# Optimization experiments

Hardware: AMD Instinct MI355X
Metric: run time of the kernel (lower is better)

Reference implementation:

```python
import jax, jax.numpy as jnp
import numpy as np


def _gru_cell(h, x, Wih, Whh, bih, bhh):
    # PyTorch GRU cell, gate order (r, z, n)
    gi = x @ Wih.T + bih      # [B, 3H]
    gh = h @ Whh.T + bhh      # [B, 3H]
    i_r, i_z, i_n = jnp.split(gi, 3, axis=-1)
    h_r, h_z, h_n = jnp.split(gh, 3, axis=-1)
    r = jax.nn.sigmoid(i_r + h_r)
    z = jax.nn.sigmoid(i_z + h_z)
    n = jnp.tanh(i_n + r * h_n)
    return (1.0 - z) * n + z * h


def _run_gru(xs, h0, Wih, Whh, bih, bhh):
    # xs: [T, B, E] -> (h_T [B, H], outputs [T, B, H])
    def step(h, x):
        h = _gru_cell(h, x, Wih, Whh, bih, bhh)
        return h, h
    return jax.lax.scan(step, h0, xs)


def setup_inputs() -> dict:
    key = jax.random.key(0)
    ks = jax.random.split(key, 14)
    V, E, H1, H2, W, C = 101, 512, 1024, 1024, 2048, 24

    def p(k, shape, fan):
        return jax.random.normal(k, shape, jnp.float32) / np.float32(np.sqrt(fan))

    return {
        "x": jax.random.randint(ks[0], (1, W, C), 0, V),
        "emb": p(ks[1], (V, E), E),
        "Wih1": p(ks[2], (3 * H1, E), E),
        "Whh1": p(ks[3], (3 * H1, H1), H1),
        "bih1": jnp.zeros((3 * H1,), jnp.float32),
        "bhh1": jnp.zeros((3 * H1,), jnp.float32),
        "Wih2f": p(ks[4], (3 * H2, H1), H1),
        "Whh2f": p(ks[5], (3 * H2, H2), H2),
        "bih2f": jnp.zeros((3 * H2,), jnp.float32),
        "bhh2f": jnp.zeros((3 * H2,), jnp.float32),
        "Wih2b": p(ks[6], (3 * H2, H1), H1),
        "Whh2b": p(ks[7], (3 * H2, H2), H2),
        "bih2b": jnp.zeros((3 * H2,), jnp.float32),
        "bhh2b": jnp.zeros((3 * H2,), jnp.float32),
    }


def reference(x, emb, Wih1, Whh1, bih1, bhh1,
              Wih2f, Whh2f, bih2f, bhh2f,
              Wih2b, Whh2b, bih2b, bhh2b):
    # x: [1, W, C] int indices. Dropout is treated as eval-mode (identity).
    Wn = x.shape[1]
    H1 = Whh1.shape[1]
    H2 = Whh2f.shape[1]

    e = emb[x[0]]                       # [W, C, E]
    xs = jnp.transpose(e, (1, 0, 2))    # [C, W, E] -- words batched together
    h0 = jnp.zeros((Wn, H1), e.dtype)
    word_emb, _ = _run_gru(xs, h0, Wih1, Whh1, bih1, bhh1)  # final hidden == last output

    # word-level bidirectional GRU, batch size 1 (the sentence)
    ws = word_emb[:, None, :]           # [W, 1, H1]
    h0w = jnp.zeros((1, H2), e.dtype)
    _, fwd = _run_gru(ws, h0w, Wih2f, Whh2f, bih2f, bhh2f)          # [W, 1, H2]
    _, bwd = _run_gru(ws[::-1], h0w, Wih2b, Whh2b, bih2b, bhh2b)    # reversed
    ctx = jnp.concatenate([fwd[:, 0, :], bwd[::-1][:, 0, :]], axis=-1)  # [W, 2*H2]

    return word_emb[None], ctx[None]    # ([1, W, H1], [1, W, 2*H2])
```

## Files before the change

### kernel.cpp

```cpp
#include <hip/hip_runtime.h>

typedef unsigned short u16;
typedef unsigned int   u32;
typedef unsigned long long u64;
typedef long long      i64;
typedef __attribute__((ext_vector_type(8))) short  short8;
typedef __attribute__((ext_vector_type(8))) __bf16 bf16x8;
typedef __attribute__((ext_vector_type(4))) float  f32x4;

#define W_N   2048
#define C_N   24
#define E_N   512
#define H_N   1024
#define G3_N  3072
#define CH    256
#define SEG   512
#define NBLK  64
#define COLS  16
#define SENT  0xFFFFFFFFu

#define MD_BF16 0u
#define MD_F32  1u
#define MD_ZERO 2u

__device__ inline float bf2f(u16 u) { union { u32 i; float f; } v; v.i = ((u32)u) << 16; return v.f; }
__device__ inline u16 f2bf(float f) {
  union { float f; u32 i; } v; v.f = f;
  u32 i = v.i;
  u32 r = (i + 0x7fffu + ((i >> 16) & 1u)) >> 16;
  return (u16)r;
}
__device__ inline float ld1(const void* p, size_t eoff, u32 md) {
  if (md == MD_F32) return ((const float*)p)[eoff];
  if (md == MD_ZERO) return 0.f;
  return bf2f(((const u16*)p)[eoff]);
}
__device__ inline short8 ld8(const void* p, size_t eoff, u32 md) {
  short8 r;
  if (md == MD_BF16) return *(const short8*)((const u16*)p + eoff);
  if (md == MD_ZERO) {
#pragma unroll
    for (int i = 0; i < 8; ++i) r[i] = 0;
    return r;
  }
  const float* f = (const float*)p + eoff;
#pragma unroll
  for (int i = 0; i < 8; ++i) r[i] = (short)f2bf(f[i]);
  return r;
}

__device__ inline void split8(f32x4 v0, f32x4 v1, bf16x8& hi, bf16x8& lo) {
#pragma unroll
  for (int i = 0; i < 4; ++i) {
    float f = v0[i];
    __bf16 h = (__bf16)f;
    hi[i] = h;
    lo[i] = (__bf16)(f - (float)h);
  }
#pragma unroll
  for (int i = 0; i < 4; ++i) {
    float f = v1[i];
    __bf16 h = (__bf16)f;
    hi[4 + i] = h;
    lo[4 + i] = (__bf16)(f - (float)h);
  }
}

__device__ inline void ldsplit(const void* p, size_t eoff, u32 md,
                               bf16x8& hi, bf16x8& lo) {
  if (md == MD_F32) {
    const float* f = (const float*)p + eoff;
    f32x4 v0 = *(const f32x4*)f;
    f32x4 v1 = *(const f32x4*)(f + 4);
    split8(v0, v1, hi, lo);
  } else if (md == MD_BF16) {
    union { short8 s; bf16x8 b; } u;
    u.s = *(const short8*)((const u16*)p + eoff);
    hi = u.b;
#pragma unroll
    for (int i = 0; i < 8; ++i) lo[i] = (__bf16)0.f;
  } else {
#pragma unroll
    for (int i = 0; i < 8; ++i) { hi[i] = (__bf16)0.f; lo[i] = (__bf16)0.f; }
  }
}

struct PtrPack { const void* p[14]; };

__global__ void sniffall_kernel(PtrPack pk, u32* __restrict__ flags) {
  if (threadIdx.x != 0) return;
  const int b = blockIdx.x;
  if (b == 0) {
    const int* xi = (const int*)pk.p[0];
    int oddzero = 0;
    for (int i = 0; i < 128; ++i)
      if (xi[2 * i + 1] == 0) oddzero++;
    flags[0] = (oddzero >= 120) ? 1u : 0u;
  } else {
    const u16* t = (const u16*)pk.p[b];
    int cnt = 0, nz = 0;
    for (int i = 0; i < 512; ++i) {
      u32 v = t[i];
      if (v != 0u) nz++;
      u32 e = (v >> 7) & 0xffu;
      if (e >= 100u && e <= 130u) cnt++;
    }
    flags[b] = (nz == 0) ? MD_ZERO : ((cnt >= 440) ? MD_BF16 : MD_F32);
  }
}

#define SWZ(row, kc) (((row) << 6) + ((kc) ^ (((row) & 7) << 3)))

template<int GATHER>
__global__ __launch_bounds__(256)
void mgemm_kernel(const void* __restrict__ A, const void* __restrict__ Wt,
                  const void* __restrict__ bias, float* __restrict__ Cout,
                  const void* __restrict__ X, int xoff, int gstride, int K,
                  const u32* __restrict__ flags, int afi, int wfi, int bfi,
                  int m_base) {
  __shared__ u16 AhS[64 * 64], AlS[64 * 64], BhS[64 * 64], BlS[64 * 64];
  __shared__ int arowS[64];
  const u32 am = (afi == -1) ? MD_BF16 : ((afi == -2) ? MD_F32 : flags[afi]);
  const u32 wm = flags[wfi];
  const u32 bm = flags[bfi];
  const int tid = threadIdx.x;
  const int bn0 = blockIdx.x * 64, bm0 = blockIdx.y * 64;
  if (GATHER) {
    if (tid < 64) {
      const int ar = m_base + bm0 + tid;
      int ix = flags[0] ? (int)((const i64*)X)[(size_t)ar * gstride + xoff]
                        : ((const int*)X)[(size_t)ar * gstride + xoff];
      arowS[tid] = min(max(ix, 0), 100);
    }
    __syncthreads();
  }
  const int wave = tid >> 6, lane = tid & 63;
  const int wr = (wave >> 1) * 32, wc = (wave & 1) * 32;
  const bool loA = (am == MD_F32), loB = (wm == MD_F32);

  f32x4 acc[2][2];
#pragma unroll
  for (int i = 0; i < 2; ++i)
#pragma unroll
    for (int j = 0; j < 2; ++j)
#pragma unroll
      for (int r = 0; r < 4; ++r) acc[i][j][r] = 0.f;

  for (int k0 = 0; k0 < K; k0 += 64) {
#pragma unroll
    for (int i = 0; i < 2; ++i) {
      const int ch = tid + i * 256;
      const int row = ch >> 3, kc = (ch & 7) * 8;
      {
        const int grow = GATHER ? arowS[row] : (m_base + bm0 + row);
        bf16x8 hi, lo;
        ldsplit(A, (size_t)grow * K + k0 + kc, am, hi, lo);
        const int o = SWZ(row, kc);
        *(bf16x8*)&AhS[o] = hi;
        *(bf16x8*)&AlS[o] = lo;
      }
      {
        bf16x8 hi, lo;
        ldsplit(Wt, (size_t)(bn0 + row) * K + k0 + kc, wm, hi, lo);
        const int o = SWZ(row, kc);
        *(bf16x8*)&BhS[o] = hi;
        *(bf16x8*)&BlS[o] = lo;
      }
    }
    __syncthreads();
#pragma unroll
    for (int ks = 0; ks < 64; ks += 32) {
      bf16x8 ah[2], al[2], bh[2], bl[2];
      const int lr = lane & 15, lk = ks + (lane >> 4) * 8;
#pragma unroll
      for (int i = 0; i < 2; ++i) {
        ah[i] = *(const bf16x8*)&AhS[SWZ(wr + i * 16 + lr, lk)];
        al[i] = *(const bf16x8*)&AlS[SWZ(wr + i * 16 + lr, lk)];
        bh[i] = *(const bf16x8*)&BhS[SWZ(wc + i * 16 + lr, lk)];
        bl[i] = *(const bf16x8*)&BlS[SWZ(wc + i * 16 + lr, lk)];
      }
#pragma unroll
      for (int i = 0; i < 2; ++i)
#pragma unroll
        for (int j = 0; j < 2; ++j) {
          acc[i][j] = __builtin_amdgcn_mfma_f32_16x16x32_bf16(ah[i], bh[j], acc[i][j], 0, 0, 0);
          if (loA)
            acc[i][j] = __builtin_amdgcn_mfma_f32_16x16x32_bf16(al[i], bh[j], acc[i][j], 0, 0, 0);
          if (loB)
            acc[i][j] = __builtin_amdgcn_mfma_f32_16x16x32_bf16(ah[i], bl[j], acc[i][j], 0, 0, 0);
        }
    }
    __syncthreads();
  }
  const int lr = lane & 15, m4 = (lane >> 4) * 4;
#pragma unroll
  for (int j = 0; j < 2; ++j) {
    const int n = bn0 + wc + j * 16 + lr;
    const float bv = ld1(bias, n, bm);
#pragma unroll
    for (int i = 0; i < 2; ++i) {
      const int m = bm0 + wr + i * 16 + m4;
#pragma unroll
      for (int r = 0; r < 4; ++r)
        Cout[(size_t)(m + r) * G3_N + n] = acc[i][j][r] + bv;
    }
  }
}

__device__ inline void seg_pass(
    const void* __restrict__ A, u32 am, int gather, const int* arowS, int bm0,
    const void* __restrict__ Wt, u32 wm, int bn0, int K,
    int tid, int wave, int lane,
    u16* AhS, u16* AlS, u16* B0h, u16* B0l, u16* B1h, u16* B1l, u16* B2h, u16* B2l,
    f32x4 (&aR)[2][2], f32x4 (&aZ)[2][2], f32x4 (&aN)[2][2]) {
  const bool loA = (am == MD_F32), loB = (wm == MD_F32);
  u16* BhS[3] = {B0h, B1h, B2h};
  u16* BlS[3] = {B0l, B1l, B2l};
  const int wr = (wave >> 1) * 32, wc = (wave & 1) * 32;
  for (int k0 = 0; k0 < K; k0 += 64) {
    __syncthreads();
#pragma unroll
    for (int i = 0; i < 2; ++i) {
      const int ch = tid + i * 256;
      const int row = ch >> 3, kc = (ch & 7) * 8;
      const int grow = gather ? arowS[row] : (bm0 + row);
      bf16x8 hi, lo;
      ldsplit(A, (size_t)grow * K + k0 + kc, am, hi, lo);
      const int o = SWZ(row, kc);
      *(bf16x8*)&AhS[o] = hi;
      *(bf16x8*)&AlS[o] = lo;
#pragma unroll
      for (int g = 0; g < 3; ++g) {
        bf16x8 bhi, blo;
        ldsplit(Wt, (size_t)(g * 1024 + bn0 + row) * K + k0 + kc, wm, bhi, blo);
        *(bf16x8*)&BhS[g][o] = bhi;
        *(bf16x8*)&BlS[g][o] = blo;
      }
    }
    __syncthreads();
#pragma unroll
    for (int ks = 0; ks < 64; ks += 32) {
      const int lr = lane & 15, lk = ks + (lane >> 4) * 8;
      bf16x8 ah[2], al[2];
#pragma unroll
      for (int i = 0; i < 2; ++i) {
        ah[i] = *(const bf16x8*)&AhS[SWZ(wr + i * 16 + lr, lk)];
        al[i] = *(const bf16x8*)&AlS[SWZ(wr + i * 16 + lr, lk)];
      }
#pragma unroll
      for (int g = 0; g < 3; ++g) {
        bf16x8 bh[2], bl[2];
#pragma unroll
        for (int j = 0; j < 2; ++j) {
          bh[j] = *(const bf16x8*)&BhS[g][SWZ(wc + j * 16 + lr, lk)];
          bl[j] = *(const bf16x8*)&BlS[g][SWZ(wc + j * 16 + lr, lk)];
        }
        f32x4 (&acc)[2][2] = (g == 0) ? aR : (g == 1) ? aZ : aN;
#pragma unroll
        for (int i = 0; i < 2; ++i)
#pragma unroll
          for (int j = 0; j < 2; ++j) {
            acc[i][j] = __builtin_amdgcn_mfma_f32_16x16x32_bf16(ah[i], bh[j], acc[i][j], 0, 0, 0);
            if (loA)
              acc[i][j] = __builtin_amdgcn_mfma_f32_16x16x32_bf16(al[i], bh[j], acc[i][j], 0, 0, 0);
            if (loB)
              acc[i][j] = __builtin_amdgcn_mfma_f32_16x16x32_bf16(ah[i], bl[j], acc[i][j], 0, 0, 0);
          }
      }
    }
  }
}

__global__ __launch_bounds__(256)
void fgru_kernel(const void* __restrict__ emb, const void* __restrict__ Wih,
                 const void* __restrict__ bih, const void* __restrict__ Whh,
                 const void* __restrict__ bhh,
                 const float* __restrict__ hin, float* __restrict__ hout,
                 float* __restrict__ wout,
                 const void* __restrict__ X, int xoff, int gstride,
                 const u32* __restrict__ flags) {
  __shared__ u16 AhS[64 * 64], AlS[64 * 64];
  __shared__ u16 B0h[64 * 64], B0l[64 * 64];
  __shared__ u16 B1h[64 * 64], B1l[64 * 64];
  __shared__ u16 B2h[64 * 64], B2l[64 * 64];
  __shared__ int arowS[64];
  const u32 amE = flags[1], wmI = flags[2], wmH = flags[3];
  const u32 bmI = flags[4], bmH = flags[5];
  const int tid = threadIdx.x, wave = tid >> 6, lane = tid & 63;
  const int bn0 = blockIdx.x * 64;
  const int bm0 = blockIdx.y * 64;
  if (tid < 64) {
    const int ar = bm0 + tid;
    int ix = flags[0] ? (int)((const i64*)X)[(size_t)ar * gstride + xoff]
                      : ((const int*)X)[(size_t)ar * gstride + xoff];
    arowS[tid] = min(max(ix, 0), 100);
  }

  f32x4 aR[2][2], aZ[2][2], aIN[2][2], aHN[2][2];
#pragma unroll
  for (int i = 0; i < 2; ++i)
#pragma unroll
    for (int j = 0; j < 2; ++j)
#pragma unroll
      for (int r = 0; r < 4; ++r) {
        aR[i][j][r] = 0.f; aZ[i][j][r] = 0.f;
        aIN[i][j][r] = 0.f; aHN[i][j][r] = 0.f;
      }

  seg_pass(emb, amE, 1, arowS, bm0, Wih, wmI, bn0, E_N,
           tid, wave, lane, AhS, AlS, B0h, B0l, B1h, B1l, B2h, B2l, aR, aZ, aIN);
  seg_pass(hin, MD_F32, 0, arowS, bm0, Whh, wmH, bn0, H_N,
           tid, wave, lane, AhS, AlS, B0h, B0l, B1h, B1l, B2h, B2l, aR, aZ, aHN);

  const int wr = (wave >> 1) * 32, wc = (wave & 1) * 32;
  const int lr = lane & 15, m4 = (lane >> 4) * 4;
#pragma unroll
  for (int j = 0; j < 2; ++j) {
    const int n = bn0 + wc + j * 16 + lr;
    const float biR = ld1(bih, n, bmI),        bhR = ld1(bhh, n, bmH);
    const float biZ = ld1(bih, 1024 + n, bmI), bhZ = ld1(bhh, 1024 + n, bmH);
    const float biN = ld1(bih, 2048 + n, bmI), bhN = ld1(bhh, 2048 + n, bmH);
#pragma unroll
    for (int i = 0; i < 2; ++i) {
      const int m = bm0 + wr + i * 16 + m4;
#pragma unroll
      for (int r4 = 0; r4 < 4; ++r4) {
        const size_t off = (size_t)(m + r4) * H_N + n;
        const float rg = 1.f / (1.f + expf(-(aR[i][j][r4] + biR + bhR)));
        const float zg = 1.f / (1.f + expf(-(aZ[i][j][r4] + biZ + bhZ)));
        const float ng = tanhf(aIN[i][j][r4] + biN + rg * (aHN[i][j][r4] + bhN));
        const float ho = (1.f - zg) * ng + zg * hin[off];
        hout[off] = ho;
        if (wout) wout[off] = ho;
      }
    }
  }
}

__global__ __launch_bounds__(256)
void gru_cell_kernel(const float* __restrict__ gi, const float* __restrict__ gh,
                     float* __restrict__ hf, float* __restrict__ wout, int mb) {
  const int idx = blockIdx.x * 256 + threadIdx.x;
  const int m = idx >> 10, j = idx & 1023;
  const float* gim = gi + (size_t)m * G3_N;
  const float* ghm = gh + (size_t)m * G3_N;
  const float ir = gim[j], iz = gim[1024 + j], inn = gim[2048 + j];
  const float hr = ghm[j], hz = ghm[1024 + j], hn = ghm[2048 + j];
  const float r = 1.f / (1.f + expf(-(ir + hr)));
  const float z = 1.f / (1.f + expf(-(iz + hz)));
  const float n = tanhf(inn + r * hn);
  const float ho = (1.f - z) * n + z * hf[idx];
  hf[idx] = ho;
  if (wout) wout[(size_t)(mb + m) * H_N + j] = ho;
}

__device__ void mgemm_body(const float* __restrict__ A, const void* __restrict__ Wt,
                           const void* __restrict__ bias, float* __restrict__ Cout,
                           u32 wm, u32 bm, int bm0, int bn0, char* smem, int tid) {
  u16* AhS = (u16*)smem;
  u16* AlS = AhS + 4096;
  u16* BhS = AlS + 4096;
  u16* BlS = BhS + 4096;
  const int wave = tid >> 6, lane = tid & 63;
  const int wr = (wave >> 1) * 32, wc = (wave & 1) * 32;
  const bool loB = (wm == MD_F32);
  const int K = H_N;

  f32x4 acc[2][2];
#pragma unroll
  for (int i = 0; i < 2; ++i)
#pragma unroll
    for (int j = 0; j < 2; ++j)
#pragma unroll
      for (int r = 0; r < 4; ++r) acc[i][j][r] = 0.f;

  for (int k0 = 0; k0 < K; k0 += 64) {
#pragma unroll
    for (int i = 0; i < 2; ++i) {
      const int ch = tid + i * 256;
      const int row = ch >> 3, kc = (ch & 7) * 8;
      {
        bf16x8 hi, lo;
        ldsplit(A, (size_t)(bm0 + row) * K + k0 + kc, MD_F32, hi, lo);
        const int o = SWZ(row, kc);
        *(bf16x8*)&AhS[o] = hi;
        *(bf16x8*)&AlS[o] = lo;
      }
      {
        bf16x8 hi, lo;
        ldsplit(Wt, (size_t)(bn0 + row) * K + k0 + kc, wm, hi, lo);
        const int o = SWZ(row, kc);
        *(bf16x8*)&BhS[o] = hi;
        *(bf16x8*)&BlS[o] = lo;
      }
    }
    __syncthreads();
#pragma unroll
    for (int ks = 0; ks < 64; ks += 32) {
      bf16x8 ah[2], al[2], bh[2], bl[2];
      const int lr = lane & 15, lk = ks + (lane >> 4) * 8;
#pragma unroll
      for (int i = 0; i < 2; ++i) {
        ah[i] = *(const bf16x8*)&AhS[SWZ(wr + i * 16 + lr, lk)];
        al[i] = *(const bf16x8*)&AlS[SWZ(wr + i * 16 + lr, lk)];
        bh[i] = *(const bf16x8*)&BhS[SWZ(wc + i * 16 + lr, lk)];
        bl[i] = *(const bf16x8*)&BlS[SWZ(wc + i * 16 + lr, lk)];
      }
#pragma unroll
      for (int i = 0; i < 2; ++i)
#pragma unroll
        for (int j = 0; j < 2; ++j) {
          acc[i][j] = __builtin_amdgcn_mfma_f32_16x16x32_bf16(ah[i], bh[j], acc[i][j], 0, 0, 0);
          acc[i][j] = __builtin_amdgcn_mfma_f32_16x16x32_bf16(al[i], bh[j], acc[i][j], 0, 0, 0);
          if (loB)
            acc[i][j] = __builtin_amdgcn_mfma_f32_16x16x32_bf16(ah[i], bl[j], acc[i][j], 0, 0, 0);
        }
    }
    __syncthreads();
  }
  const int lr = lane & 15, m4 = (lane >> 4) * 4;
#pragma unroll
  for (int j = 0; j < 2; ++j) {
    const int n = bn0 + wc + j * 16 + lr;
    const float bv = ld1(bias, n, bm);
#pragma unroll
    for (int i = 0; i < 2; ++i) {
      const int m = bm0 + wr + i * 16 + m4;
#pragma unroll
      for (int r = 0; r < 4; ++r) {
        union { float f; u32 u; } cv; cv.f = acc[i][j][r] + bv;
        __hip_atomic_store((u32*)Cout + (size_t)(m + r) * G3_N + n, cv.u,
                           __ATOMIC_RELAXED, __HIP_MEMORY_SCOPE_AGENT);
      }
    }
  }
}

__device__ void seq_body(const void* __restrict__ Whh, const void* __restrict__ bhh,
                         const float* __restrict__ gi, float* __restrict__ ctx,
                         u32 wm, u32 bm, int dir, int blk, char* smem, int tid,
                         int nsteps) {
  u16* wsh = (u16*)smem;
  const int dirofs = dir << 10;
  const int wave = tid >> 6, lane = tid & 63;
  const int j0 = blk * COLS;
  const int jw = wave * 4;

  for (int e = tid * 8; e < 48 * 1024; e += 256 * 8) {
    const int lr = e >> 10, col = e & 1023;
    const int g = lr >> 4, jj = lr & 15;
    *(short8*)&wsh[e] = ld8(Whh, (size_t)(g * 1024 + j0 + jj) * 1024 + col, wm);
  }
  float br = 0.f, bz = 0.f, bn = 0.f;
  if (lane < 4) {
    br = ld1(bhh, 0 * 1024 + j0 + jw + lane, bm);
    bz = ld1(bhh, 1 * 1024 + j0 + jw + lane, bm);
    bn = ld1(bhh, 2 * 1024 + j0 + jw + lane, bm);
  }
  __syncthreads();

  float hp = 0.f;
  for (int t = 0; t < nsteps; ++t) {
    const int row = dir ? (nsteps - 1 - t) : t;
    u32 ga = 0, gb = 0, gc = 0;
    {
      const u32* gp = (const u32*)(gi + (size_t)row * G3_N + (j0 + jw + (lane & 3)));
      for (;;) {
        if (lane < 4) {
          ga = __hip_atomic_load(gp,        __ATOMIC_RELAXED, __HIP_MEMORY_SCOPE_AGENT);
          gb = __hip_atomic_load(gp + 1024, __ATOMIC_RELAXED, __HIP_MEMORY_SCOPE_AGENT);
          gc = __hip_atomic_load(gp + 2048, __ATOMIC_RELAXED, __HIP_MEMORY_SCOPE_AGENT);
        }
        const bool bad = (lane < 4) && (ga == SENT || gb == SENT || gc == SENT);
        if (__ballot(bad) == 0ull) break;
      }
    }
    union { u32 u; float f; } c0, c1, c2;
    c0.u = ga; c1.u = gb; c2.u = gc;
    const float ir = c0.f, iz = c1.f, inn = c2.f;

    float hreg[16];
    if (t == 0) {
#pragma unroll
      for (int i = 0; i < 16; ++i) hreg[i] = 0.f;
    } else {
      const int prow = dir ? (nsteps - t) : (t - 1);
      const u64* hsrc = (const u64*)(ctx + (size_t)prow * 2048 + dirofs);
      u64 hv[8];
      for (;;) {
        bool bad = false;
#pragma unroll
        for (int c = 0; c < 8; ++c) {
          hv[c] = __hip_atomic_load(hsrc + c * 64 + lane,
                                    __ATOMIC_RELAXED, __HIP_MEMORY_SCOPE_AGENT);
          if ((u32)hv[c] == SENT || (u32)(hv[c] >> 32) == SENT)
            bad = true;
        }
        if (__ballot(bad) == 0ull) break;
      }
#pragma unroll
      for (int c = 0; c < 8; ++c) {
        union { u64 u; float f[2]; } cv; cv.u = hv[c];
        hreg[2 * c]     = cv.f[0];
        hreg[2 * c + 1] = cv.f[1];
      }
    }
    float sv[12];
#pragma unroll
    for (int g = 0; g < 3; ++g)
#pragma unroll
      for (int jj = 0; jj < 4; ++jj) {
        const u32* wrow = (const u32*)&wsh[(g * 16 + jw + jj) * 1024];
        float s = 0.f;
#pragma unroll
        for (int c = 0; c < 8; ++c) {
          const u32 u = wrow[c * 64 + lane];
          union { u32 i; float f; } lo2, hi2;
          lo2.i = u << 16; hi2.i = u & 0xffff0000u;
          s = fmaf(lo2.f, hreg[2 * c], s);
          s = fmaf(hi2.f, hreg[2 * c + 1], s);
        }
#pragma unroll
        for (int off = 32; off > 0; off >>= 1) s += __shfl_xor(s, off);
        sv[g * 4 + jj] = s;
      }
    if (lane < 4) {
      const float hr = (lane == 0 ? sv[0] : lane == 1 ? sv[1] : lane == 2 ? sv[2] : sv[3]) + br;
      const float hz = (lane == 0 ? sv[4] : lane == 1 ? sv[5] : lane == 2 ? sv[6] : sv[7]) + bz;
      const float hn = (lane == 0 ? sv[8] : lane == 1 ? sv[9] : lane == 2 ? sv[10] : sv[11]) + bn;
      const float r = 1.f / (1.f + expf(-(ir + hr)));
      const float z = 1.f / (1.f + expf(-(iz + hz)));
      const float n = tanhf(inn + r * hn);
      const float ho = (1.f - z) * n + z * hp;
      hp = ho;
      union { float f; u32 i; } v; v.f = ho;
      __hip_atomic_store((u32*)(ctx + (size_t)row * 2048) + dirofs + j0 + jw + lane,
                         v.i, __ATOMIC_RELAXED, __HIP_MEMORY_SCOPE_AGENT);
    }
  }
}

__global__ __launch_bounds__(256)
void p2_kernel(const void* __restrict__ Whf, const void* __restrict__ bhf,
               const void* __restrict__ Whb, const void* __restrict__ bhb,
               const void* __restrict__ Wif, const void* __restrict__ bif,
               const void* __restrict__ Wib, const void* __restrict__ bib,
               const float* __restrict__ wemb, float* __restrict__ G0,
               float* __restrict__ G1, float* __restrict__ ctx,
               const u32* __restrict__ flags, int nsteps) {
  __shared__ __align__(16) char smem[48 * 1024 * 2];
  const int tid = threadIdx.x;
  const int bid = blockIdx.x;
  if (bid < 2 * NBLK) {
    const int dir = bid >> 6, blk = bid & 63;
    seq_body(dir ? Whb : Whf, dir ? bhb : bhf, dir ? G1 : G0, ctx,
             flags[dir ? 11 : 7], flags[dir ? 13 : 9], dir, blk, smem, tid, nsteps);
  } else {
    int b = bid - 2 * NBLK;
    if (b < 1536) {
      const int bx = b % 48, by = b / 48;
      mgemm_body(wemb, Wif, bif, G0, flags[6], flags[8], by * 64, bx * 64, smem, tid);
    } else {
      b -= 1536;
      const int bx = b % 48, by = 31 - (b / 48);
      mgemm_body(wemb, Wib, bib, G1, flags[10], flags[12], by * 64, bx * 64, smem, tid);
    }
  }
}

__global__ __launch_bounds__(256)
void seq_kernel(const void* __restrict__ Whh, const void* __restrict__ bhh,
                const float* __restrict__ gi, float* hb, unsigned* cnt,
                float* __restrict__ ctx, const u32* __restrict__ flags,
                int wfi, int bfi, int word_base, int rev, int dirofs) {
  const u32 wm = flags[wfi], bm = flags[bfi];
  const int blk = blockIdx.x;
  const int tid = threadIdx.x;
  const int wave = tid >> 6, lane = tid & 63;
  const int j0 = blk * 8;

  __shared__ __align__(16) u16 wsh[24 * 1024];
  __shared__ float hshf[1024];
  __shared__ float ghs[24];
  __shared__ float bhs[24];
  __shared__ float hnew[8];

  for (int e = tid * 8; e < 24 * 1024; e += 256 * 8) {
    const int lr = e >> 10, col = e & 1023;
    const int g = lr >> 3, jj = lr & 7;
    *(short8*)&wsh[e] = ld8(Whh, (size_t)(g * 1024 + j0 + jj) * 1024 + col, wm);
  }
  if (tid < 24) bhs[tid] = ld1(bhh, (tid >> 3) * 1024 + j0 + (tid & 7), bm);
  __syncthreads();

  unsigned target = 0;
  for (int t = 0; t < SEG; ++t) {
    const int row = rev ? (SEG - 1 - t) : t;
    const int wt = word_base + row;
    const u32* hsrc = (const u32*)(hb + (t & 1) * 1024);
    u32* hdst = (u32*)hshf;
    if (wave == 0) {
#pragma unroll
      for (int c = 0; c < 16; ++c)
        hdst[c * 64 + lane] = __hip_atomic_load(hsrc + c * 64 + lane,
                                                __ATOMIC_RELAXED, __HIP_MEMORY_SCOPE_AGENT);
    }
    __syncthreads();
    float hreg[16];
#pragma unroll
    for (int c = 0; c < 8; ++c) {
      const int kp = 2 * (c * 64 + lane);
      hreg[2 * c]     = hshf[kp];
      hreg[2 * c + 1] = hshf[kp + 1];
    }
#pragma unroll
    for (int q = 0; q < 6; ++q) {
      const int lr = wave * 6 + q;
      const u32* wrow = (const u32*)&wsh[lr * 1024];
      float s = 0.f;
#pragma unroll
      for (int c = 0; c < 8; ++c) {
        const u32 u = wrow[c * 64 + lane];
        union { u32 i; float f; } lo, hi;
        lo.i = u << 16; hi.i = u & 0xffff0000u;
        s = fmaf(lo.f, hreg[2 * c], s);
        s = fmaf(hi.f, hreg[2 * c + 1], s);
      }
#pragma unroll
      for (int off = 32; off > 0; off >>= 1) s += __shfl_xor(s, off);
      if (lane == 0) ghs[lr] = s;
    }
    __syncthreads();
    if (tid < 8) {
      const int jj = tid;
      const float hr = ghs[jj] + bhs[jj];
      const float hz = ghs[8 + jj] + bhs[8 + jj];
      const float hn = ghs[16 + jj] + bhs[16 + jj];
      const float* gim = gi + (size_t)row * G3_N + (j0 + jj);
      const float ir = gim[0], iz = gim[1024], inn = gim[2048];
      const float r = 1.f / (1.f + expf(-(ir + hr)));
      const float z = 1.f / (1.f + expf(-(iz + hz)));
      const float n = tanhf(inn + r * hn);
      const float hp = hshf[j0 + jj];
      const float ho = (1.f - z) * n + z * hp;
      ctx[(size_t)wt * 2048 + dirofs + j0 + jj] = ho;
      hnew[jj] = ho;
    }
    __syncthreads();
    if (tid < 8) {
      union { float f; u32 i; } v; v.f = hnew[tid];
      __hip_atomic_store((u32*)(hb + ((t + 1) & 1) * 1024) + blk * 8 + tid, v.i,
                         __ATOMIC_RELAXED, __HIP_MEMORY_SCOPE_AGENT);
    }
    target += 128;
    if (tid == 0) {
      __hip_atomic_fetch_add(cnt, 1u, __ATOMIC_RELEASE, __HIP_MEMORY_SCOPE_AGENT);
      while (__hip_atomic_load(cnt, __ATOMIC_ACQUIRE, __HIP_MEMORY_SCOPE_AGENT) < target)
        __builtin_amdgcn_s_sleep(2);
    }
    __syncthreads();
  }
}

extern "C" void kernel_launch(void* const* d_in, const int* in_sizes, int n_in,
                              void* d_out, int out_size, void* d_ws, size_t ws_size,
                              hipStream_t stream) {
  char* w = (char*)d_ws;
  u32* flags = (u32*)(w);
  float* hbuf = (float*)(w + 1024);
  const size_t GBASE = 20480;

  hipMemsetAsync(w, 0, GBASE, stream);

  PtrPack pk;
  for (int i = 0; i < 14; ++i) pk.p[i] = d_in[i];
  sniffall_kernel<<<14, 64, 0, stream>>>(pk, flags);

  float* wemb = (float*)d_out;
  float* ctx  = (float*)d_out + (size_t)W_N * H_N;

  const size_t SZ_G  = (size_t)W_N * G3_N * 4;
  const size_t SZ_HF = (size_t)W_N * H_N * 4;
  const size_t needA = GBASE + 2 * SZ_G + SZ_HF;

  if (ws_size >= needA) {
    float* G0 = (float*)(w + GBASE);
    float* G1 = (float*)(w + GBASE + SZ_G);
    float* HA = (float*)(w + GBASE + 2 * SZ_G);
    float* HB = G0;

    hipMemsetAsync(HA, 0, SZ_HF, stream);

    float* bufs[2] = {HA, HB};
    dim3 gf(H_N / 64, W_N / 64);
    for (int c = 0; c < C_N; ++c) {
      fgru_kernel<<<gf, 256, 0, stream>>>(d_in[1], d_in[2], d_in[4], d_in[3], d_in[5],
                                          bufs[c & 1], bufs[(c + 1) & 1],
                                          (c == C_N - 1) ? wemb : (float*)nullptr,
                                          d_in[0], c, C_N, flags);
    }

    hipMemsetAsync(G0, 0xFF, SZ_G, stream);
    hipMemsetAsync(G1, 0xFF, SZ_G, stream);
    hipMemsetAsync(ctx, 0xFF, (size_t)W_N * 2048 * 4, stream);

    p2_kernel<<<2 * NBLK + 2 * 1536, 256, 0, stream>>>(
        d_in[7], d_in[9], d_in[11], d_in[13],
        d_in[6], d_in[8], d_in[10], d_in[12],
        wemb, G0, G1, ctx, flags, W_N);
  } else {
    float* G0  = (float*)(w + GBASE);
    float* GIc = G0;
    float* GHc = G0 + (size_t)CH * G3_N;
    float* HF  = (float*)(w + GBASE + (size_t)SEG * G3_N * 4);

    dim3 g1(G3_N / 64, CH / 64);
    for (int chk = 0; chk < W_N / CH; ++chk) {
      const int mb = chk * CH;
      hipMemsetAsync(HF, 0, (size_t)CH * H_N * 4, stream);
      for (int c = 0; c < C_N; ++c) {
        mgemm_kernel<1><<<g1, 256, 0, stream>>>(d_in[1], d_in[2], d_in[4], GIc,
                                                d_in[0], c, C_N, E_N, flags, 1, 2, 4, mb);
        mgemm_kernel<0><<<g1, 256, 0, stream>>>(HF, d_in[3], d_in[5], GHc,
                                                nullptr, 0, 0, H_N, flags, -2, 3, 5, 0);
        gru_cell_kernel<<<(CH * H_N) / 256, 256, 0, stream>>>(
            GIc, GHc, HF, (c == C_N - 1) ? wemb : (float*)nullptr, mb);
      }
    }
    dim3 g2(G3_N / 64, SEG / 64);
    for (int s = 0; s < W_N / SEG; ++s) {
      mgemm_kernel<0><<<g2, 256, 0, stream>>>(wemb, d_in[6], d_in[8], G0,
                                              nullptr, 0, 0, H_N, flags, -2, 6, 8, s * SEG);
      seq_kernel<<<128, 256, 0, stream>>>(d_in[7], d_in[9], G0, hbuf,
                                          (unsigned*)(w + 64 + (0 * 4 + s) * 64),
                                          ctx, flags, 7, 9, s * SEG, 0, 0);
    }
    for (int s = W_N / SEG - 1; s >= 0; --s) {
      mgemm_kernel<0><<<g2, 256, 0, stream>>>(wemb, d_in[10], d_in[12], G0,
                                              nullptr, 0, 0, H_N, flags, -2, 10, 12, s * SEG);
      seq_kernel<<<128, 256, 0, stream>>>(d_in[11], d_in[13], G0, hbuf + 2048,
                                          (unsigned*)(w + 64 + (1 * 4 + s) * 64),
                                          ctx, flags, 11, 13, s * SEG, 1, 1024);
    }
  }
}
```

Measured before the change: 9.880 ms.

## Precompute embedding-input projection table over vocabulary and gather it per step

Since the vocabulary has only 101 entries, the input projection emb·Wih^T + bih is computed once into a 128x3072 table by a gather-mode GEMM. Each of the 24 char-level GRU steps then looks up rows of this table instead of redoing a K=512 GEMM against the embedding. This removes roughly a third of the per-step matrix work and the Wih weight streaming. In exchange it adds one small GEMM launch and scattered table reads in the epilogue.

```diff
diff --git a/kernel.cpp b/kernel.cpp
--- a/kernel.cpp
+++ b/kernel.cpp
@@ -128,8 +128,10 @@
   if (GATHER) {
     if (tid < 64) {
       const int ar = m_base + bm0 + tid;
-      int ix = flags[0] ? (int)((const i64*)X)[(size_t)ar * gstride + xoff]
-                        : ((const int*)X)[(size_t)ar * gstride + xoff];
+      int ix;
+      if (GATHER == 2) ix = ar;
+      else ix = flags[0] ? (int)((const i64*)X)[(size_t)ar * gstride + xoff]
+                         : ((const int*)X)[(size_t)ar * gstride + xoff];
       arowS[tid] = min(max(ix, 0), 100);
     }
     __syncthreads();
@@ -208,7 +210,7 @@
 }
 
 __device__ inline void seg_pass(
-    const void* __restrict__ A, u32 am, int gather, const int* arowS, int bm0,
+    const void* __restrict__ A, u32 am, int bm0,
     const void* __restrict__ Wt, u32 wm, int bn0, int K,
     int tid, int wave, int lane,
     u16* AhS, u16* AlS, u16* B0h, u16* B0l, u16* B1h, u16* B1l, u16* B2h, u16* B2l,
@@ -223,9 +225,8 @@
     for (int i = 0; i < 2; ++i) {
       const int ch = tid + i * 256;
       const int row = ch >> 3, kc = (ch & 7) * 8;
-      const int grow = gather ? arowS[row] : (bm0 + row);
       bf16x8 hi, lo;
-      ldsplit(A, (size_t)grow * K + k0 + kc, am, hi, lo);
+      ldsplit(A, (size_t)(bm0 + row) * K + k0 + kc, am, hi, lo);
       const int o = SWZ(row, kc);
       *(bf16x8*)&AhS[o] = hi;
       *(bf16x8*)&AlS[o] = lo;
@@ -272,8 +273,7 @@
 }
 
 __global__ __launch_bounds__(256)
-void fgru_kernel(const void* __restrict__ emb, const void* __restrict__ Wih,
-                 const void* __restrict__ bih, const void* __restrict__ Whh,
+void fgru_kernel(const float* __restrict__ P, const void* __restrict__ Whh,
                  const void* __restrict__ bhh,
                  const float* __restrict__ hin, float* __restrict__ hout,
                  float* __restrict__ wout,
@@ -284,8 +284,7 @@
   __shared__ u16 B1h[64 * 64], B1l[64 * 64];
   __shared__ u16 B2h[64 * 64], B2l[64 * 64];
   __shared__ int arowS[64];
-  const u32 amE = flags[1], wmI = flags[2], wmH = flags[3];
-  const u32 bmI = flags[4], bmH = flags[5];
+  const u32 wmH = flags[3], bmH = flags[5];
   const int tid = threadIdx.x, wave = tid >> 6, lane = tid & 63;
   const int bn0 = blockIdx.x * 64;
   const int bm0 = blockIdx.y * 64;
@@ -296,20 +295,17 @@
     arowS[tid] = min(max(ix, 0), 100);
   }
 
-  f32x4 aR[2][2], aZ[2][2], aIN[2][2], aHN[2][2];
+  f32x4 aR[2][2], aZ[2][2], aHN[2][2];
 #pragma unroll
   for (int i = 0; i < 2; ++i)
 #pragma unroll
     for (int j = 0; j < 2; ++j)
 #pragma unroll
       for (int r = 0; r < 4; ++r) {
-        aR[i][j][r] = 0.f; aZ[i][j][r] = 0.f;
-        aIN[i][j][r] = 0.f; aHN[i][j][r] = 0.f;
-      }
-
-  seg_pass(emb, amE, 1, arowS, bm0, Wih, wmI, bn0, E_N,
-           tid, wave, lane, AhS, AlS, B0h, B0l, B1h, B1l, B2h, B2l, aR, aZ, aIN);
-  seg_pass(hin, MD_F32, 0, arowS, bm0, Whh, wmH, bn0, H_N,
+        aR[i][j][r] = 0.f; aZ[i][j][r] = 0.f; aHN[i][j][r] = 0.f;
+      }
+
+  seg_pass(hin, MD_F32, bm0, Whh, wmH, bn0, H_N,
            tid, wave, lane, AhS, AlS, B0h, B0l, B1h, B1l, B2h, B2l, aR, aZ, aHN);
 
   const int wr = (wave >> 1) * 32, wc = (wave & 1) * 32;
@@ -317,18 +313,19 @@
 #pragma unroll
   for (int j = 0; j < 2; ++j) {
     const int n = bn0 + wc + j * 16 + lr;
-    const float biR = ld1(bih, n, bmI),        bhR = ld1(bhh, n, bmH);
-    const float biZ = ld1(bih, 1024 + n, bmI), bhZ = ld1(bhh, 1024 + n, bmH);
-    const float biN = ld1(bih, 2048 + n, bmI), bhN = ld1(bhh, 2048 + n, bmH);
+    const float bhR = ld1(bhh, n, bmH);
+    const float bhZ = ld1(bhh, 1024 + n, bmH);
+    const float bhN = ld1(bhh, 2048 + n, bmH);
 #pragma unroll
     for (int i = 0; i < 2; ++i) {
-      const int m = bm0 + wr + i * 16 + m4;
+      const int lm = wr + i * 16 + m4;
 #pragma unroll
       for (int r4 = 0; r4 < 4; ++r4) {
-        const size_t off = (size_t)(m + r4) * H_N + n;
-        const float rg = 1.f / (1.f + expf(-(aR[i][j][r4] + biR + bhR)));
-        const float zg = 1.f / (1.f + expf(-(aZ[i][j][r4] + biZ + bhZ)));
-        const float ng = tanhf(aIN[i][j][r4] + biN + rg * (aHN[i][j][r4] + bhN));
+        const size_t off = (size_t)(bm0 + lm + r4) * H_N + n;
+        const float* Pr = P + (size_t)arowS[lm + r4] * G3_N + n;
+        const float rg = 1.f / (1.f + expf(-(Pr[0]    + aR[i][j][r4] + bhR)));
+        const float zg = 1.f / (1.f + expf(-(Pr[1024] + aZ[i][j][r4] + bhZ)));
+        const float ng = tanhf(Pr[2048] + rg * (aHN[i][j][r4] + bhN));
         const float ho = (1.f - zg) * ng + zg * hin[off];
         hout[off] = ho;
         if (wout) wout[off] = ho;
@@ -679,22 +676,27 @@
   float* wemb = (float*)d_out;
   float* ctx  = (float*)d_out + (size_t)W_N * H_N;
 
+  const size_t SZ_P  = (size_t)128 * G3_N * 4;
   const size_t SZ_G  = (size_t)W_N * G3_N * 4;
   const size_t SZ_HF = (size_t)W_N * H_N * 4;
-  const size_t needA = GBASE + 2 * SZ_G + SZ_HF;
+  const size_t needA = GBASE + SZ_P + 2 * SZ_G + SZ_HF;
 
   if (ws_size >= needA) {
-    float* G0 = (float*)(w + GBASE);
-    float* G1 = (float*)(w + GBASE + SZ_G);
-    float* HA = (float*)(w + GBASE + 2 * SZ_G);
+    float* P  = (float*)(w + GBASE);
+    float* G0 = (float*)(w + GBASE + SZ_P);
+    float* G1 = G0 + (size_t)W_N * G3_N;
+    float* HA = G1 + (size_t)W_N * G3_N;
     float* HB = G0;
 
     hipMemsetAsync(HA, 0, SZ_HF, stream);
+
+    mgemm_kernel<2><<<dim3(G3_N / 64, 2), 256, 0, stream>>>(
+        d_in[1], d_in[2], d_in[4], P, nullptr, 0, 0, E_N, flags, 1, 2, 4, 0);
 
     float* bufs[2] = {HA, HB};
     dim3 gf(H_N / 64, W_N / 64);
     for (int c = 0; c < C_N; ++c) {
-      fgru_kernel<<<gf, 256, 0, stream>>>(d_in[1], d_in[2], d_in[4], d_in[3], d_in[5],
+      fgru_kernel<<<gf, 256, 0, stream>>>(P, d_in[3], d_in[5],
                                           bufs[c & 1], bufs[(c + 1) & 1],
                                           (c == C_N - 1) ? wemb : (float*)nullptr,
                                           d_in[0], c, C_N, flags);
```

Result: faster. 9.129 ms (-7.6%).
